# Optimization experiments

Measured on AMD Instinct MI355X. Metric: run time of the kernel, lower is better.

Reference implementation:

```python
import jax, jax.numpy as jnp
import numpy as np

WS = [2048, 4096, 8192]
RS = [1, 2, 4]
OFFSET = 0
NEG = -1e30


def _causal_attn(xseg, Wq, Wk, Wv, Wo):
    """xseg: (b, s, m, c). Returns (out (b,s,m,c), denom (b,s,m)) where denom is
    the softmax denominator sum_j exp(score_ij) per query (computed stably via lse)."""
    c = xseg.shape[-1]
    m = xseg.shape[-2]
    q = jnp.einsum('bsmc,cd->bsmd', xseg, Wq)
    k = jnp.einsum('bsmc,cd->bsmd', xseg, Wk)
    v = jnp.einsum('bsmc,cd->bsmd', xseg, Wv)
    scores = jnp.einsum('bsid,bsjd->bsij', q, k) / jnp.sqrt(jnp.asarray(c, xseg.dtype))
    causal = jnp.tril(jnp.ones((m, m), dtype=bool))
    scores = jnp.where(causal, scores, NEG)
    lse = jax.nn.logsumexp(scores, axis=-1)            # (b,s,m)
    p = jnp.exp(scores - lse[..., None])               # softmax
    o = jnp.einsum('bsij,bsjd->bsid', p, v)
    o = jnp.einsum('bsid,dc->bsic', o, Wo)
    return o, jnp.exp(lse)


def setup_inputs() -> dict:
    key = jax.random.key(0)
    kx, kq, kk, kv, ko = jax.random.split(key, 5)
    b, n, c = 4, 8192, 128
    scale = 1.0 / np.sqrt(c)  # keep activations O(1) so exp(lse) stays finite
    return {
        'x': jax.random.normal(kx, (b, n, c), dtype=jnp.float32),
        'Wq': jax.random.normal(kq, (c, c), dtype=jnp.float32) * scale,
        'Wk': jax.random.normal(kk, (c, c), dtype=jnp.float32) * scale,
        'Wv': jax.random.normal(kv, (c, c), dtype=jnp.float32) * scale,
        'Wo': jax.random.normal(ko, (c, c), dtype=jnp.float32) * scale,
    }


def reference(x, Wq, Wk, Wv, Wo):
    b, n, c = x.shape
    denom_sums = jnp.zeros((b, n), dtype=x.dtype)
    branches = []
    for w, r in zip(WS, RS):
        s = n // w
        # gather dilated tokens within each segment: (b, s, m, c)
        xr = x.reshape(b, s, w, c)[:, :, OFFSET::r, :]
        m = xr.shape[2]
        o, d = _causal_attn(xr, Wq, Wk, Wv, Wo)
        # global positions of the gathered tokens, flattened over (segment, within-seg)
        idx = (jnp.arange(s)[:, None] * w + OFFSET + r * jnp.arange(m)[None, :]).reshape(-1)
        d_flat = d.reshape(b, s * m)
        o_flat = o.reshape(b, s * m, c)
        denom_sums = denom_sums.at[:, idx].add(d_flat)
        branches.append((idx, o_flat, d_flat))
    out = jnp.zeros_like(x)
    for idx, o_flat, d_flat in branches:
        alpha = d_flat / denom_sums[:, idx]             # (b, s*m)
        out = out.at[:, idx].add(o_flat * alpha[..., None])
    return out
```

## Files before the change

kernel.cpp:

```cpp
#include <hip/hip_runtime.h>
#include <hip/hip_bf16.h>

typedef __attribute__((ext_vector_type(8))) __bf16 bf16x8;
typedef __attribute__((ext_vector_type(4))) float f32x4;
typedef __attribute__((ext_vector_type(8))) unsigned short u16x8;

#define DEVI __device__ __forceinline__
#define MFMA(a,b,c) __builtin_amdgcn_mfma_f32_16x16x32_bf16((a),(b),(c),0,0,0)
#define EXP2F(x) __builtin_exp2f(x)
#define LOG2F(x) __builtin_log2f(x)

DEVI unsigned short f2bf(float f){ __bf16 h = (__bf16)f; return __builtin_bit_cast(unsigned short, h); }
DEVI float bf2f(unsigned short u){ unsigned int x = ((unsigned int)u) << 16; return __builtin_bit_cast(float, x); }
DEVI bf16x8 ld_bf8(const void* p){ u16x8 u = *(const u16x8*)p; return __builtin_bit_cast(bf16x8, u); }
DEVI f32x4 splat4(float x){ f32x4 v = {x,x,x,x}; return v; }
DEVI f32x4 vmax4(f32x4 a, f32x4 b){
  f32x4 r;
  #pragma unroll
  for (int i=0;i<4;++i) r[i]=fmaxf(a[i],b[i]);
  return r;
}
DEVI void gload_lds16(const void* g, void* l){
  void* g2 = const_cast<void*>(g);
  __builtin_amdgcn_global_load_lds((__attribute__((address_space(1))) void*)g2,
                                   (__attribute__((address_space(3))) void*)l, 16, 0, 0);
}
#if __has_builtin(__builtin_amdgcn_permlane16_swap) && __has_builtin(__builtin_amdgcn_permlane32_swap)
DEVI float wavemax_hi(float x){
  unsigned int xu = __builtin_bit_cast(unsigned int, x);
  auto r1 = __builtin_amdgcn_permlane16_swap(xu, xu, false, false);
  float m = fmaxf(__builtin_bit_cast(float, (unsigned int)r1[0]),
                  __builtin_bit_cast(float, (unsigned int)r1[1]));
  unsigned int mu = __builtin_bit_cast(unsigned int, m);
  auto r2 = __builtin_amdgcn_permlane32_swap(mu, mu, false, false);
  return fmaxf(__builtin_bit_cast(float, (unsigned int)r2[0]),
               __builtin_bit_cast(float, (unsigned int)r2[1]));
}
#else
DEVI float wavemax_hi(float x){
  x = fmaxf(x, __shfl_xor(x, 16, 64));
  x = fmaxf(x, __shfl_xor(x, 32, 64));
  return x;
}
#endif

__device__ const unsigned int SCHED[30] = {
  0x100C000Bu, 0x110C0C0Bu, 0x050C0005u, 0x1C0B0A0Fu, 0x1D0B150Fu,
  0x0E0B000Au, 0x0F0B0B0Au, 0x1B0A000Fu, 0x180A000Eu, 0x190A0A0Eu,
  0x1A0A140Eu, 0x170A120Du, 0x0C0A0009u, 0x0D0A0A09u, 0x040A0004u,
  0x1509000Du, 0x1609090Du, 0x1309080Cu, 0x1409110Cu, 0x0A090008u,
  0x0B090908u, 0x1208000Cu, 0x08080007u, 0x09080807u, 0x03080003u,
  0x06070006u, 0x07070706u, 0x02060002u, 0x01040001u, 0x00020000u
};
__device__ const int CB[16] = {0,1,2,3,4,5,6,8,10,12,14,16,18,21,24,27};

__global__ __launch_bounds__(256) void k_prep(const float* __restrict__ Wq, const float* __restrict__ Wk,
                                              const float* __restrict__ Wv, const float* __restrict__ Wo,
                                              unsigned short* __restrict__ wT){
  int i = blockIdx.x*256 + threadIdx.x;
  int mat = i >> 14, col = (i >> 7) & 127, k = i & 127;
  const float* W = (mat==0)?Wq:(mat==1)?Wk:(mat==2)?Wv:Wo;
  float v = W[k*128 + col];
  if (mat == 0) v *= 0.12754245006257017f;
  wT[i] = f2bf(v);
}

__global__ __launch_bounds__(256) void k_qkv(const float* __restrict__ x, const unsigned short* __restrict__ wT,
                                             unsigned short* __restrict__ Qo, unsigned short* __restrict__ Ko,
                                             unsigned short* __restrict__ VT0, unsigned short* __restrict__ VT1,
                                             unsigned short* __restrict__ VT2){
  __shared__ unsigned short Tl[128*130];
  const int tid=threadIdx.x, lane=tid&63, wid=tid>>6, ll=lane&15, hi=lane>>4;
  const int row0g = blockIdx.x*128;
  const long row0 = (long)row0g + wid*32;
  bf16x8 a[2][4];
  #pragma unroll
  for (int mt=0;mt<2;++mt){
    const float* xr = x + (row0 + mt*16 + ll)*128 + hi*8;
    #pragma unroll
    for (int ks=0;ks<4;++ks){
      f32x4 f0 = *(const f32x4*)(const void*)(xr + ks*32);
      f32x4 f1 = *(const f32x4*)(const void*)(xr + ks*32 + 4);
      u16x8 u;
      #pragma unroll
      for (int j=0;j<4;++j){ u[j]=f2bf(f0[j]); u[j+4]=f2bf(f1[j]); }
      a[mt][ks] = __builtin_bit_cast(bf16x8, u);
    }
  }
  #pragma unroll
  for (int m3=0;m3<3;++m3){
    const unsigned short* wp = wT + m3*16384 + ll*128 + hi*8;
    #pragma unroll
    for (int nt=0;nt<8;++nt){
      f32x4 acc0=splat4(0.f), acc1=splat4(0.f);
      #pragma unroll
      for (int ks=0;ks<4;++ks){
        bf16x8 b = ld_bf8(wp + nt*2048 + ks*32);
        acc0 = MFMA(a[0][ks], b, acc0);
        acc1 = MFMA(a[1][ks], b, acc1);
      }
      if (m3 < 2){
        unsigned short* outp = (m3==0)?Qo:Ko;
        #pragma unroll
        for (int r=0;r<4;++r){
          outp[(row0 + hi*4 + r)*128 + nt*16 + ll]      = f2bf(acc0[r]);
          outp[(row0 + 16 + hi*4 + r)*128 + nt*16 + ll] = f2bf(acc1[r]);
        }
      } else {
        #pragma unroll
        for (int r=0;r<4;++r){
          Tl[(wid*32 + hi*4 + r)*130 + nt*16 + ll]      = f2bf(acc0[r]);
          Tl[(wid*32 + 16 + hi*4 + r)*130 + nt*16 + ll] = f2bf(acc1[r]);
        }
      }
    }
  }
  __syncthreads();
  int tk = 2*lane;
  int pp0 = (tk>>5)*32 + ((tk>>4)&1)*4 + ((tk&15)>>2)*8 + (tk&3);
  #pragma unroll 4
  for (int p=0;p<32;++p){
    int d = wid*32 + p;
    unsigned int w0 = (unsigned int)Tl[(2*lane)*130 + d] | ((unsigned int)Tl[(2*lane+1)*130 + d] << 16);
    *(unsigned int*)(VT0 + (long)d*32768 + row0g + pp0) = w0;
    if (lane < 32){
      unsigned int w1 = (unsigned int)Tl[(4*lane)*130 + d] | ((unsigned int)Tl[(4*lane+2)*130 + d] << 16);
      *(unsigned int*)(VT1 + (long)d*16384 + (row0g>>1) + pp0) = w1;
    }
    if (lane < 16){
      unsigned int w2 = (unsigned int)Tl[(8*lane)*130 + d] | ((unsigned int)Tl[(8*lane+4)*130 + d] << 16);
      *(unsigned int*)(VT2 + (long)d*8192 + (row0g>>2) + pp0) = w2;
    }
  }
}

__global__ __launch_bounds__(256,3) void k_attn(
    const unsigned short* __restrict__ Qg, const unsigned short* __restrict__ Kg,
    const unsigned short* __restrict__ VT0, const unsigned short* __restrict__ VT1,
    const unsigned short* __restrict__ VT2,
    unsigned short* __restrict__ OP, float* __restrict__ LP){
  __shared__ unsigned char smem[49152];

  const int tid=threadIdx.x, lane=tid&63, wid=tid>>6, ll=lane&15, hi=lane>>4;

  int x = blockIdx.x & 7;
  int i = blockIdx.x >> 3;
  int sid, r;
  if (i < 60){
    r = i >> 2; int k = i & 3;
    if (k < 3){ sid = 3*x + k; }
    else { sid = 24 + (x >> 1); if (x & 1) r += 15; }
  } else {
    int t = i - 60; r = 15 + t/3; sid = 3*x + t%3;
  }
  unsigned int e = SCHED[r];
  int qb   = (int)(e & 255u);
  int t032 = (int)((e >> 8) & 255u) * 2;
  int n32  = (int)((e >> 16) & 255u) * 2;
  int slot = (int)(e >> 24);
  int br, bb, seg;
  if (sid < 16){ br=0; bb=sid>>2; seg=sid&3; }
  else if (sid < 24){ br=1; bb=(sid-16)>>1; seg=(sid-16)&1; }
  else { br=2; bb=sid-24; seg=0; }
  const int rstr = 1 << br;
  const long g0 = (long)bb*8192 + (long)seg*(2048 << br);
  const int P = sid*30 + slot;
  const unsigned short* VTb = (br==0)?VT0:(br==1)?VT1:VT2;
  const int NC = 32768 >> br;
  const int rb0 = (int)(g0 >> br);

  const int qrow_w = qb*128 + wid*32;

  bf16x8 aq[2][4];
  #pragma unroll
  for (int mt=0;mt<2;++mt){
    long gq = g0 + (long)rstr*(qrow_w + mt*16 + ll);
    const unsigned short* qp = Qg + gq*128 + hi*8;
    #pragma unroll
    for (int ks=0;ks<4;++ks) aq[mt][ks] = ld_bf8(qp + ks*32);
  }

  f32x4 o[2][8];
  #pragma unroll
  for (int mt=0;mt<2;++mt){
    #pragma unroll
    for (int dt=0;dt<8;++dt) o[mt][dt]=splat4(0.f);
  }
  float mrun[2], lrun[2];
  mrun[0]=mrun[1]=-1e30f; lrun[0]=lrun[1]=0.f;

  const int m7 = ll & 7;
  int koffs[4];
  #pragma unroll
  for (int ks=0;ks<4;++ks) koffs[ks] = ll*256 + (((ks*4 + hi) ^ m7) * 16);
  const int voffb = ll*64 + (((hi + (ll >> 1)) & 3) * 16);

  const long kadv = (long)rstr*32*128;
  const unsigned short* ksrc0 = Kg + (g0 + (long)rstr*((long)t032*32 + wid*8 + hi))*128 + ((ll ^ hi) * 8);
  const unsigned short* ksrc1 = Kg + (g0 + (long)rstr*((long)t032*32 + wid*8 + 4 + hi))*128 + ((ll ^ (4 + hi)) * 8);
  const int d0_ = tid >> 2,        s0_ = tid & 3,        ga_ = (s0_ - (d0_ >> 1)) & 3;
  const int d1_ = (256+tid) >> 2,  s1_ = tid & 3,        gb_ = (s1_ - (d1_ >> 1)) & 3;
  const unsigned short* vsrc0 = VTb + (long)d0_*NC + rb0 + t032*32 + ga_*8;
  const unsigned short* vsrc1 = VTb + (long)d1_*NC + rb0 + t032*32 + gb_*8;

#define STAGE(bslot)                                                                   \
  {                                                                                    \
    unsigned char* Kb = smem + (bslot)*8192;                                           \
    unsigned char* Vb = smem + 24576 + (bslot)*8192;                                   \
    gload_lds16((const void*)ksrc0, (void*)(Kb + wid*2048));                           \
    gload_lds16((const void*)ksrc1, (void*)(Kb + wid*2048 + 1024));                    \
    gload_lds16((const void*)vsrc0, (void*)(Vb + wid*1024));                           \
    gload_lds16((const void*)vsrc1, (void*)(Vb + 4096 + wid*1024));                    \
    ksrc0 += kadv; ksrc1 += kadv; vsrc0 += 32; vsrc1 += 32;                            \
  }

  STAGE(0);
  STAGE(1);

  for (int it=0; it<n32; ++it){
    const int kt = t032 + it;
    if (it + 1 < n32){
      asm volatile("s_waitcnt vmcnt(4) lgkmcnt(0)" ::: "memory");
    } else {
      asm volatile("s_waitcnt vmcnt(0) lgkmcnt(0)" ::: "memory");
    }
    __builtin_amdgcn_s_barrier();
    __builtin_amdgcn_sched_barrier(0);

    if (it + 2 < n32){
      STAGE((it + 2) % 3);
    }

    if (kt*32 <= qrow_w + 31){
      unsigned char* Kc = smem + (it % 3)*8192;
      unsigned char* Vc = smem + 24576 + (it % 3)*8192;
      f32x4 s[2][2];
      #pragma unroll
      for (int mt=0;mt<2;++mt){
        #pragma unroll
        for (int nt=0;nt<2;++nt) s[mt][nt]=splat4(0.f);
      }
      #pragma unroll
      for (int nt=0;nt<2;++nt){
        #pragma unroll
        for (int ks=0;ks<4;++ks){
          bf16x8 bk = ld_bf8(Kc + koffs[ks] + nt*4096);
          s[0][nt] = MFMA(bk, aq[0][ks], s[0][nt]);
          s[1][nt] = MFMA(bk, aq[1][ks], s[1][nt]);
        }
      }
      if (kt*32 + 31 > qrow_w){
        #pragma unroll
        for (int mt=0;mt<2;++mt){
          int qrow = qrow_w + mt*16 + ll;
          #pragma unroll
          for (int nt=0;nt<2;++nt){
            int kvcol = kt*32 + nt*16 + hi*4;
            #pragma unroll
            for (int rr=0;rr<4;++rr) if (kvcol + rr > qrow) s[mt][nt][rr] = -1e30f;
          }
        }
      }
      #pragma unroll
      for (int mt=0;mt<2;++mt){
        f32x4 t4 = vmax4(s[mt][0], s[mt][1]);
        float mloc = fmaxf(fmaxf(t4[0],t4[1]), fmaxf(t4[2],t4[3]));
        mloc = wavemax_hi(mloc);
        bool upd = __any(mloc > mrun[mt] + 8.0f);
        if (upd){
          float mnew = fmaxf(mrun[mt], mloc);
          float sc = EXP2F(mrun[mt] - mnew);
          mrun[mt] = mnew;
          lrun[mt] *= sc;
          f32x4 scv;
          #pragma unroll
          for (int rr=0;rr<4;++rr) scv[rr] = __shfl(sc, hi*4 + rr, 64);
          #pragma unroll
          for (int dt=0;dt<8;++dt) o[mt][dt] = o[mt][dt]*scv;
        }
        f32x4 tsum = splat4(0.f);
        #pragma unroll
        for (int nt=0;nt<2;++nt){
          #pragma unroll
          for (int rr=0;rr<4;++rr) s[mt][nt][rr] = EXP2F(s[mt][nt][rr] - mrun[mt]);
          tsum += s[mt][nt];
        }
        lrun[mt] += (tsum[0]+tsum[1]) + (tsum[2]+tsum[3]);
      }
      bf16x8 pa[2];
      #pragma unroll
      for (int mt=0;mt<2;++mt){
        u16x8 up;
        #pragma unroll
        for (int rr=0;rr<4;++rr){
          up[rr]   = f2bf(s[mt][0][rr]);
          up[4+rr] = f2bf(s[mt][1][rr]);
        }
        pa[mt] = __builtin_bit_cast(bf16x8, up);
      }
      #pragma unroll
      for (int dt=0;dt<8;++dt){
        bf16x8 bv = ld_bf8(Vc + voffb + dt*1024);
        o[0][dt] = MFMA(pa[0], bv, o[0][dt]);
        o[1][dt] = MFMA(pa[1], bv, o[1][dt]);
      }
    }
  }
#undef STAGE

  unsigned short* op = OP + (long)P*16384;
  float* lp = LP + (long)P*128;
  #pragma unroll
  for (int mt=0;mt<2;++mt){
    float l = lrun[mt];
    l += __shfl_xor(l, 16, 64);
    l += __shfl_xor(l, 32, 64);
    float invs = 1.f / l;
    f32x4 iv;
    #pragma unroll
    for (int rr=0;rr<4;++rr) iv[rr] = __shfl(invs, hi*4 + rr, 64);
    #pragma unroll
    for (int dt=0;dt<8;++dt){
      f32x4 res = o[mt][dt]*iv;
      #pragma unroll
      for (int rr=0;rr<4;++rr){
        int qloc = wid*32 + mt*16 + hi*4 + rr;
        op[qloc*128 + dt*16 + ll] = f2bf(res[rr]);
      }
    }
    float lse = mrun[mt] + LOG2F(l);
    if (lane < 16){
      lp[wid*32 + mt*16 + lane] = lse;
    }
  }
}

__global__ __launch_bounds__(256) void k_comb(
    const unsigned short* __restrict__ OP, const float* __restrict__ LP,
    const unsigned short* __restrict__ wT, float* __restrict__ out){
  const int tid=threadIdx.x, lane=tid&63, wid=tid>>6, ll=lane&15, hi=lane>>4;
  const long row0 = (long)blockIdx.x*128 + wid*32;
  bf16x8 a[2][4];
  #pragma unroll
  for (int mt=0;mt<2;++mt){
    int g = (int)(row0 + mt*16 + ll);
    int bb = g >> 13;
    int posn = g & 8191;
    bool bv[3]; int pbase[3]; int ql[3]; int bn[3];
    {
      int sid = bb*4 + (posn >> 11);
      int qrow = posn & 2047;
      int qb = qrow >> 7;
      bv[0]=true; ql[0]=qrow & 127; bn[0]=(qb<6)?1:(qb<12)?2:3; pbase[0]=sid*30 + CB[qb];
    }
    if ((posn & 1) == 0){
      int p1 = posn >> 1;
      int sid = 16 + bb*2 + (p1 >> 11);
      int qrow = p1 & 2047;
      int qb = qrow >> 7;
      bv[1]=true; ql[1]=qrow & 127; bn[1]=(qb<6)?1:(qb<12)?2:3; pbase[1]=sid*30 + CB[qb];
    } else { bv[1]=false; ql[1]=0; bn[1]=0; pbase[1]=0; }
    if ((posn & 3) == 0){
      int p2 = posn >> 2;
      int sid = 24 + bb;
      int qb = p2 >> 7;
      bv[2]=true; ql[2]=p2 & 127; bn[2]=(qb<6)?1:(qb<12)?2:3; pbase[2]=sid*30 + CB[qb];
    } else { bv[2]=false; ql[2]=0; bn[2]=0; pbase[2]=0; }

    float Lx[3][3];
    #pragma unroll
    for (int b=0;b<3;++b){
      #pragma unroll
      for (int c=0;c<3;++c){
        bool v = bv[b] && (c < bn[b]);
        Lx[b][c] = v ? LP[(pbase[b]+c)*128 + ql[b]] : -1e30f;
      }
    }
    float mx = -1e30f;
    #pragma unroll
    for (int b=0;b<3;++b){
      #pragma unroll
      for (int c=0;c<3;++c) mx = fmaxf(mx, Lx[b][c]);
    }
    float W[3][3]; float wsum = 0.f;
    #pragma unroll
    for (int b=0;b<3;++b){
      #pragma unroll
      for (int c=0;c<3;++c){
        bool v = bv[b] && (c < bn[b]);
        W[b][c] = v ? EXP2F(Lx[b][c] - mx) : 0.f;
        wsum += W[b][c];
      }
    }
    float inv = 1.f / wsum;

    float y[4][8];
    #pragma unroll
    for (int ks=0;ks<4;++ks){
      #pragma unroll
      for (int jj=0;jj<8;++jj) y[ks][jj]=0.f;
    }
    #pragma unroll
    for (int b=0;b<3;++b){
      #pragma unroll
      for (int c=0;c<3;++c){
        if (bv[b] && (c < bn[b])){
          const unsigned short* p = OP + (long)(pbase[b]+c)*16384 + ql[b]*128 + hi*8;
          float wgt = W[b][c];
          #pragma unroll
          for (int ks=0;ks<4;++ks){
            u16x8 u = *(const u16x8*)(const void*)(p + ks*32);
            #pragma unroll
            for (int jj=0;jj<8;++jj) y[ks][jj] += wgt * bf2f(u[jj]);
          }
        }
      }
    }
    #pragma unroll
    for (int ks=0;ks<4;++ks){
      u16x8 u;
      #pragma unroll
      for (int jj=0;jj<8;++jj) u[jj] = f2bf(y[ks][jj]*inv);
      a[mt][ks] = __builtin_bit_cast(bf16x8, u);
    }
  }
  const unsigned short* wp = wT + 3*16384 + ll*128 + hi*8;
  #pragma unroll
  for (int nt=0;nt<8;++nt){
    f32x4 acc0=splat4(0.f), acc1=splat4(0.f);
    #pragma unroll
    for (int ks=0;ks<4;++ks){
      bf16x8 b = ld_bf8(wp + nt*2048 + ks*32);
      acc0 = MFMA(a[0][ks], b, acc0);
      acc1 = MFMA(a[1][ks], b, acc1);
    }
    #pragma unroll
    for (int rr=0;rr<4;++rr){
      out[(row0 + hi*4 + rr)*128 + nt*16 + ll] = acc0[rr];
      out[(row0 + 16 + hi*4 + rr)*128 + nt*16 + ll] = acc1[rr];
    }
  }
}

extern "C" void kernel_launch(void* const* d_in, const int* in_sizes, int n_in,
                              void* d_out, int out_size, void* d_ws, size_t ws_size,
                              hipStream_t stream){
  const float* x  = (const float*)d_in[0];
  const float* Wq = (const float*)d_in[1];
  const float* Wk = (const float*)d_in[2];
  const float* Wv = (const float*)d_in[3];
  const float* Wo = (const float*)d_in[4];
  char* ws = (char*)d_ws;
  unsigned short* wT  = (unsigned short*)(ws);
  unsigned short* Q   = (unsigned short*)(ws + 131072);
  unsigned short* K   = (unsigned short*)(ws + 8519680);
  unsigned short* VT0 = (unsigned short*)(ws + 16908288);
  unsigned short* VT1 = (unsigned short*)(ws + 25296896);
  unsigned short* VT2 = (unsigned short*)(ws + 29491200);
  unsigned short* OP  = (unsigned short*)(ws + 31588352);
  float* LP           = (float*)(ws + 59113472);
  k_prep<<<256, 256, 0, stream>>>(Wq, Wk, Wv, Wo, wT);
  k_qkv <<<256, 256, 0, stream>>>(x, wT, Q, K, VT0, VT1, VT2);
  k_attn<<<840, 256, 0, stream>>>(Q, K, VT0, VT1, VT2, OP, LP);
  k_comb<<<256, 256, 0, stream>>>(OP, LP, wT, (float*)d_out);
}
```

Before: 109.1 us.

## Restructure combine kernel: 32 rows per block with LDS-staged weights and tiles

The combine kernel now handles 32 output rows per block instead of 128 and launches 1024 blocks instead of 256. Within a block, 32 threads compute the branch mixing weights into shared memory. All 256 threads then gather and blend the partial outputs with coalesced 16-byte loads, one channel chunk per thread, and stage the bf16 result in LDS. A single wavefront performs the Wo projection with MFMA. The aim is more parallelism and better-coalesced gathers in the combine stage, at the cost of two barriers and most threads sitting idle during the MFMA phase.

```diff
diff --git a/kernel.cpp b/kernel.cpp
--- a/kernel.cpp
+++ b/kernel.cpp
@@ -338,106 +338,110 @@
 __global__ __launch_bounds__(256) void k_comb(
     const unsigned short* __restrict__ OP, const float* __restrict__ LP,
     const unsigned short* __restrict__ wT, float* __restrict__ out){
-  const int tid=threadIdx.x, lane=tid&63, wid=tid>>6, ll=lane&15, hi=lane>>4;
-  const long row0 = (long)blockIdx.x*128 + wid*32;
-  bf16x8 a[2][4];
-  #pragma unroll
-  for (int mt=0;mt<2;++mt){
-    int g = (int)(row0 + mt*16 + ll);
-    int bb = g >> 13;
-    int posn = g & 8191;
-    bool bv[3]; int pbase[3]; int ql[3]; int bn[3];
-    {
-      int sid = bb*4 + (posn >> 11);
-      int qrow = posn & 2047;
-      int qb = qrow >> 7;
-      bv[0]=true; ql[0]=qrow & 127; bn[0]=(qb<6)?1:(qb<12)?2:3; pbase[0]=sid*30 + CB[qb];
-    }
-    if ((posn & 1) == 0){
-      int p1 = posn >> 1;
-      int sid = 16 + bb*2 + (p1 >> 11);
-      int qrow = p1 & 2047;
-      int qb = qrow >> 7;
-      bv[1]=true; ql[1]=qrow & 127; bn[1]=(qb<6)?1:(qb<12)?2:3; pbase[1]=sid*30 + CB[qb];
-    } else { bv[1]=false; ql[1]=0; bn[1]=0; pbase[1]=0; }
-    if ((posn & 3) == 0){
-      int p2 = posn >> 2;
-      int sid = 24 + bb;
-      int qb = p2 >> 7;
-      bv[2]=true; ql[2]=p2 & 127; bn[2]=(qb<6)?1:(qb<12)?2:3; pbase[2]=sid*30 + CB[qb];
-    } else { bv[2]=false; ql[2]=0; bn[2]=0; pbase[2]=0; }
-
-    float Lx[3][3];
+  __shared__ float Wl[9*32];
+  __shared__ unsigned short Tl[32*136];
+  const int tid = threadIdx.x;
+  const long G0 = (long)blockIdx.x * 32;
+  const int bb = (int)(G0 >> 13);
+  const int P0 = (int)(G0 & 8191);
+
+  int pb[3], bn[3], qlb[3];
+  {
+    int sid0 = bb*4 + (P0 >> 11); int qb0 = (P0 & 2047) >> 7;
+    pb[0] = sid0*30 + CB[qb0]; bn[0] = (qb0<6)?1:(qb0<12)?2:3; qlb[0] = P0 & 127;
+    int p1b = P0 >> 1; int sid1 = 16 + bb*2 + (p1b >> 11); int qb1 = (p1b & 2047) >> 7;
+    pb[1] = sid1*30 + CB[qb1]; bn[1] = (qb1<6)?1:(qb1<12)?2:3; qlb[1] = p1b & 127;
+    int p2b = P0 >> 2; int sid2 = 24 + bb; int qb2 = p2b >> 7;
+    pb[2] = sid2*30 + CB[qb2]; bn[2] = (qb2<6)?1:(qb2<12)?2:3; qlb[2] = p2b & 127;
+  }
+
+  if (tid < 32){
+    int i = tid;
+    float Lx[9];
     #pragma unroll
     for (int b=0;b<3;++b){
+      bool pv = (i & ((1<<b)-1)) == 0;
+      int ql = qlb[b] + (i >> b);
       #pragma unroll
       for (int c=0;c<3;++c){
-        bool v = bv[b] && (c < bn[b]);
-        Lx[b][c] = v ? LP[(pbase[b]+c)*128 + ql[b]] : -1e30f;
+        bool v = pv && (c < bn[b]);
+        Lx[b*3+c] = v ? LP[(pb[b]+c)*128 + ql] : -1e30f;
       }
     }
     float mx = -1e30f;
     #pragma unroll
+    for (int s=0;s<9;++s) mx = fmaxf(mx, Lx[s]);
+    float W[9]; float wsum = 0.f;
+    #pragma unroll
     for (int b=0;b<3;++b){
-      #pragma unroll
-      for (int c=0;c<3;++c) mx = fmaxf(mx, Lx[b][c]);
-    }
-    float W[3][3]; float wsum = 0.f;
-    #pragma unroll
-    for (int b=0;b<3;++b){
+      bool pv = (i & ((1<<b)-1)) == 0;
       #pragma unroll
       for (int c=0;c<3;++c){
-        bool v = bv[b] && (c < bn[b]);
-        W[b][c] = v ? EXP2F(Lx[b][c] - mx) : 0.f;
-        wsum += W[b][c];
+        bool v = pv && (c < bn[b]);
+        W[b*3+c] = v ? EXP2F(Lx[b*3+c] - mx) : 0.f;
+        wsum += W[b*3+c];
       }
     }
     float inv = 1.f / wsum;
-
-    float y[4][8];
-    #pragma unroll
-    for (int ks=0;ks<4;++ks){
-      #pragma unroll
-      for (int jj=0;jj<8;++jj) y[ks][jj]=0.f;
-    }
-    #pragma unroll
-    for (int b=0;b<3;++b){
-      #pragma unroll
-      for (int c=0;c<3;++c){
-        if (bv[b] && (c < bn[b])){
-          const unsigned short* p = OP + (long)(pbase[b]+c)*16384 + ql[b]*128 + hi*8;
-          float wgt = W[b][c];
-          #pragma unroll
-          for (int ks=0;ks<4;++ks){
-            u16x8 u = *(const u16x8*)(const void*)(p + ks*32);
+    #pragma unroll
+    for (int s=0;s<9;++s) Wl[s*32 + i] = W[s] * inv;
+  }
+  __syncthreads();
+
+  {
+    const int ch = tid & 15;
+    const int r0 = tid >> 4;
+    #pragma unroll
+    for (int p=0;p<2;++p){
+      int row = p*16 + r0;
+      float y[8];
+      #pragma unroll
+      for (int j=0;j<8;++j) y[j] = 0.f;
+      #pragma unroll
+      for (int b=0;b<3;++b){
+        if ((row & ((1<<b)-1)) == 0){
+          int opr = qlb[b] + (row >> b);
+          for (int c=0;c<bn[b];++c){
+            float wgt = Wl[(b*3+c)*32 + row];
+            const unsigned short* pp = OP + (long)(pb[b]+c)*16384 + opr*128 + ch*8;
+            u16x8 u = *(const u16x8*)(const void*)pp;
             #pragma unroll
-            for (int jj=0;jj<8;++jj) y[ks][jj] += wgt * bf2f(u[jj]);
+            for (int j=0;j<8;++j) y[j] += wgt * bf2f(u[j]);
           }
         }
       }
-    }
-    #pragma unroll
-    for (int ks=0;ks<4;++ks){
-      u16x8 u;
-      #pragma unroll
-      for (int jj=0;jj<8;++jj) u[jj] = f2bf(y[ks][jj]*inv);
-      a[mt][ks] = __builtin_bit_cast(bf16x8, u);
-    }
-  }
-  const unsigned short* wp = wT + 3*16384 + ll*128 + hi*8;
-  #pragma unroll
-  for (int nt=0;nt<8;++nt){
-    f32x4 acc0=splat4(0.f), acc1=splat4(0.f);
-    #pragma unroll
-    for (int ks=0;ks<4;++ks){
-      bf16x8 b = ld_bf8(wp + nt*2048 + ks*32);
-      acc0 = MFMA(a[0][ks], b, acc0);
-      acc1 = MFMA(a[1][ks], b, acc1);
-    }
-    #pragma unroll
-    for (int rr=0;rr<4;++rr){
-      out[(row0 + hi*4 + rr)*128 + nt*16 + ll] = acc0[rr];
-      out[(row0 + 16 + hi*4 + rr)*128 + nt*16 + ll] = acc1[rr];
+      u16x8 o;
+      #pragma unroll
+      for (int j=0;j<8;++j) o[j] = f2bf(y[j]);
+      *(u16x8*)(void*)(Tl + row*136 + ch*8) = o;
+    }
+  }
+  __syncthreads();
+
+  if (tid < 64){
+    const int lane = tid, ll = lane & 15, hi = lane >> 4;
+    bf16x8 a[2][4];
+    #pragma unroll
+    for (int mt=0;mt<2;++mt){
+      #pragma unroll
+      for (int ks=0;ks<4;++ks)
+        a[mt][ks] = ld_bf8(Tl + (mt*16 + ll)*136 + ks*32 + hi*8);
+    }
+    const unsigned short* wp = wT + 3*16384 + ll*128 + hi*8;
+    #pragma unroll
+    for (int nt=0;nt<8;++nt){
+      f32x4 acc0=splat4(0.f), acc1=splat4(0.f);
+      #pragma unroll
+      for (int ks=0;ks<4;++ks){
+        bf16x8 b = ld_bf8(wp + nt*2048 + ks*32);
+        acc0 = MFMA(a[0][ks], b, acc0);
+        acc1 = MFMA(a[1][ks], b, acc1);
+      }
+      #pragma unroll
+      for (int rr=0;rr<4;++rr){
+        out[(G0 + hi*4 + rr)*128 + nt*16 + ll]      = acc0[rr];
+        out[(G0 + 16 + hi*4 + rr)*128 + nt*16 + ll] = acc1[rr];
+      }
     }
   }
 }
@@ -462,5 +466,5 @@
   k_prep<<<256, 256, 0, stream>>>(Wq, Wk, Wv, Wo, wT);
   k_qkv <<<256, 256, 0, stream>>>(x, wT, Q, K, VT0, VT1, VT2);
   k_attn<<<840, 256, 0, stream>>>(Q, K, VT0, VT1, VT2, OP, LP);
-  k_comb<<<256, 256, 0, stream>>>(OP, LP, wT, (float*)d_out);
-}
+  k_comb<<<1024, 256, 0, stream>>>(OP, LP, wT, (float*)d_out);
+}
```

Result: faster. 105.6 us (-3.2%).
